# Optimization experiments

Hardware: AMD Instinct MI355X
Metric: run time of the kernel (lower is better)

Reference implementation:

```python
import jax, jax.numpy as jnp
import numpy as np

N, L, D1, D2, K, C, T = 50000, 1024, 512, 256, 64, 2, 49


def setup_inputs() -> dict:
    key = jax.random.key(0)
    ks = jax.random.split(key, 20)
    s = 0.02
    return {
        "h": jax.random.normal(ks[0], (N, L), dtype=jnp.float32),
        "tabular": jax.random.normal(ks[1], (1, T), dtype=jnp.float32),
        "label": 1,
        # fc: Linear(1024,512)+ReLU
        "W_fc": jax.random.normal(ks[2], (L, D1)) * s, "b_fc": jnp.zeros((D1,)),
        # gated attention net
        "Wa": jax.random.normal(ks[3], (D1, D2)) * s, "ba": jnp.zeros((D2,)),
        "Wb": jax.random.normal(ks[4], (D1, D2)) * s, "bb": jnp.zeros((D2,)),
        "Wc": jax.random.normal(ks[5], (D2, 1)) * s, "bc": jnp.zeros((1,)),
        # per-class instance classifiers Linear(512,2), stacked [C, D1, 2]
        "W_inst": jax.random.normal(ks[6], (C, D1, 2)) * s, "b_inst": jnp.zeros((C, 2)),
        # MultiHeadAttention (1 head)
        "W_img": jax.random.normal(ks[7], (D1, 1)) * s, "b_img": jnp.zeros((1,)),
        "W_tab": jax.random.normal(ks[8], (T, T)) * s, "b_tab": jnp.zeros((T,)),
        # bag classifier Linear(512+49, 2)
        "W_cls": jax.random.normal(ks[9], (D1 + T, C)) * s, "b_cls": jnp.zeros((C,)),
    }


def _forward(h, tabular, label, W_fc, b_fc, Wa, ba, Wb, bb, Wc, bc,
             W_inst, b_inst, W_img, b_img, W_tab, b_tab, W_cls, b_cls):
    # attention_net: fc + ReLU then gated attention
    h512 = jax.nn.relu(h @ W_fc + b_fc)                       # [N, 512]
    a = jnp.tanh(h512 @ Wa + ba)                              # [N, 256]
    b = jax.nn.sigmoid(h512 @ Wb + bb)                        # [N, 256]
    A = ((a * b) @ Wc + bc).T                                 # [1, N]
    A_raw = A
    A = jax.nn.softmax(A, axis=1)                             # [1, N]

    # instance eval: top-k positive / top-k negative selection + tiny classifier + CE
    scores = A[0]                                             # [N]
    _, top_p_ids = jax.lax.top_k(scores, K)
    _, top_n_ids = jax.lax.top_k(-scores, K)
    all_inst = jnp.concatenate([h512[top_p_ids], h512[top_n_ids]], axis=0)  # [2K, 512]
    targets = jnp.concatenate([jnp.ones((K,), jnp.int32), jnp.zeros((K,), jnp.int32)])

    def inst_loss(Wi, bi):
        logits = all_inst @ Wi + bi                           # [2K, 2]
        logp = jax.nn.log_softmax(logits, axis=1)
        return -jnp.mean(logp[jnp.arange(2 * K), targets])

    losses = jax.vmap(inst_loss)(W_inst, b_inst)              # [C]
    onehot = jax.nn.one_hot(label, C, dtype=losses.dtype)
    total_inst_loss = jnp.sum(onehot * losses)                # only in-class classifier contributes

    # attention pooling
    M = A @ h512                                              # [1, 512]

    # MultiHeadAttention (1 head): gated image feature + softmax-gated tabular feature
    img_score = jax.nn.sigmoid(M @ W_img + b_img)             # [1, 1]
    tab_score = jax.nn.softmax(tabular @ W_tab + b_tab, axis=1)  # [1, 49]
    concat = jnp.concatenate([img_score * M, tab_score * tabular], axis=1)  # [1, 561]

    logits = concat @ W_cls + b_cls                           # [1, 2]
    Y_prob = jax.nn.softmax(logits, axis=1)
    Y_hat = jnp.argmax(logits, axis=1)
    return logits, Y_prob, Y_hat, A_raw, total_inst_loss


def reference(h, tabular, label, W_fc, b_fc, Wa, ba, Wb, bb, Wc, bc,
              W_inst, b_inst, W_img, b_img, W_tab, b_tab, W_cls, b_cls):
    return _forward(h, tabular, label, W_fc, b_fc, Wa, ba, Wb, bb, Wc, bc,
                    W_inst, b_inst, W_img, b_img, W_tab, b_tab, W_cls, b_cls)
```

## Files before the change

kernel.cpp:

```cpp
#include <hip/hip_runtime.h>
#include <stdint.h>

typedef __bf16 bf16x8 __attribute__((ext_vector_type(8)));
typedef float f32x4 __attribute__((ext_vector_type(4)));
typedef unsigned short u16;
typedef unsigned int u32;

#define N_INST 50000
#define NPAD   50048
#define LIN    1024
#define D1     512
#define D2     256
#define TOPK   64
#define TDIM   49
#define NBIN   65536
#define CAND_MAX 8192
#define ZERO_DW (520 + 128 + 16 + NBIN)

__device__ __forceinline__ float b2f(u16 u) {
    union { float f; u32 i; } x; x.i = ((u32)u) << 16; return x.f;
}
__device__ __forceinline__ u16 f2b(float f) {
    union { float f; u32 i; } x; x.f = f;
    u32 r = x.i + 0x7FFFu + ((x.i >> 16) & 1u);
    return (u16)(r >> 16);
}
__device__ __forceinline__ void gload16(const void* g, void* l) {
    __builtin_amdgcn_global_load_lds((const __attribute__((address_space(1))) void*)g,
                                     (__attribute__((address_space(3))) void*)l, 16, 0, 0);
}

__global__ void pack_w(const float* __restrict__ W_fc, const float* __restrict__ Wa,
                       const float* __restrict__ Wb, u16* __restrict__ WfcT,
                       u16* __restrict__ WaT, u16* __restrict__ WbT, u32* __restrict__ zbase) {
    int gt = blockIdx.x * blockDim.x + threadIdx.x;
    int nthr = gridDim.x * blockDim.x;
    for (int z = gt; z < ZERO_DW; z += nthr) zbase[z] = 0u;
    for (int e = gt; e < D1 * LIN; e += nthr) {
        int n = e >> 10, k = e & 1023;
        WfcT[e] = f2b(W_fc[(size_t)k * D1 + n]);
    }
    for (int f = gt; f < D2 * D1; f += nthr) {
        int j = f >> 9, k = f & 511;
        WaT[f] = f2b(Wa[(size_t)k * D2 + j]);
        WbT[f] = f2b(Wb[(size_t)k * D2 + j]);
    }
}

__global__ __launch_bounds__(512, 2)
void gemm_fc(const float* __restrict__ h, const u16* __restrict__ WfcT,
             const float* __restrict__ b_fc, u16* __restrict__ h512) {
    __shared__ __align__(16) u16 lA[128 * 64];
    __shared__ __align__(16) u16 lB[512 * 64];
    const int tid = threadIdx.x;
    const int lane = tid & 63, wid = tid >> 6;
    const int wr = wid >> 2, wc = wid & 3;
    const int lanelo = lane & 15, lanehi = lane >> 4;
    const int row0 = blockIdx.x * 128;

    const int arow = tid >> 2;
    const int aseg = tid & 3;
    int srow = row0 + arow; if (srow >= N_INST) srow = N_INST - 1;
    const float* abase = h + (size_t)srow * LIN + aseg * 16;

    f32x4 acc[4][8];
    const f32x4 z4 = {0.f, 0.f, 0.f, 0.f};
    #pragma unroll
    for (int m = 0; m < 4; ++m)
        #pragma unroll
        for (int n = 0; n < 8; ++n) acc[m][n] = z4;

    for (int kt = 0; kt < LIN / 64; ++kt) {
        #pragma unroll
        for (int q = 0; q < 8; ++q) {
            int c = tid + 512 * q;
            int col = c >> 3, k8 = c & 7;
            gload16(WfcT + (size_t)col * LIN + kt * 64 + k8 * 8, (char*)lB + c * 16);
        }
        {
            const float4* ap = (const float4*)(abase + kt * 64);
            float4 a0 = ap[0], a1 = ap[1], a2 = ap[2], a3 = ap[3];
            bf16x8 w0, w1;
            w0[0] = (__bf16)a0.x; w0[1] = (__bf16)a0.y; w0[2] = (__bf16)a0.z; w0[3] = (__bf16)a0.w;
            w0[4] = (__bf16)a1.x; w0[5] = (__bf16)a1.y; w0[6] = (__bf16)a1.z; w0[7] = (__bf16)a1.w;
            w1[0] = (__bf16)a2.x; w1[1] = (__bf16)a2.y; w1[2] = (__bf16)a2.z; w1[3] = (__bf16)a2.w;
            w1[4] = (__bf16)a3.x; w1[5] = (__bf16)a3.y; w1[6] = (__bf16)a3.z; w1[7] = (__bf16)a3.w;
            *(bf16x8*)(lA + arow * 64 + aseg * 16) = w0;
            *(bf16x8*)(lA + arow * 64 + aseg * 16 + 8) = w1;
        }
        __syncthreads();
        #pragma unroll
        for (int kk = 0; kk < 2; ++kk) {
            bf16x8 af[4], bfr[8];
            #pragma unroll
            for (int m = 0; m < 4; ++m)
                af[m] = *(const bf16x8*)((char*)lA + (wr * 64 + m * 16 + lanelo) * 128 + kk * 64 + lanehi * 16);
            #pragma unroll
            for (int n = 0; n < 8; ++n)
                bfr[n] = *(const bf16x8*)((char*)lB + (wc * 128 + n * 16 + lanelo) * 128 + kk * 64 + lanehi * 16);
            #pragma unroll
            for (int m = 0; m < 4; ++m)
                #pragma unroll
                for (int n = 0; n < 8; ++n)
                    acc[m][n] = __builtin_amdgcn_mfma_f32_16x16x32_bf16(af[m], bfr[n], acc[m][n], 0, 0, 0);
        }
        __syncthreads();
    }
    #pragma unroll
    for (int n = 0; n < 8; ++n) {
        int col = wc * 128 + n * 16 + lanelo;
        float bias = b_fc[col];
        #pragma unroll
        for (int m = 0; m < 4; ++m) {
            int rbase = row0 + wr * 64 + m * 16 + 4 * lanehi;
            #pragma unroll
            for (int r = 0; r < 4; ++r) {
                float v = acc[m][n][r] + bias;
                v = v > 0.f ? v : 0.f;
                h512[(size_t)(rbase + r) * D1 + col] = f2b(v);
            }
        }
    }
}

__global__ __launch_bounds__(512, 2)
void gemm_attn(const u16* __restrict__ h512, const u16* __restrict__ WaT,
               const u16* __restrict__ WbT, const float* __restrict__ ba,
               const float* __restrict__ bb, const float* __restrict__ Wc,
               const float* __restrict__ bc, float* __restrict__ araw,
               u32* __restrict__ uarr, u32* __restrict__ hist,
               float* __restrict__ Zacc, float* __restrict__ Mpart) {
    __shared__ __align__(16) u16 lA[128 * 64];
    __shared__ __align__(16) u16 lBa[256 * 64];
    __shared__ __align__(16) u16 lBb[256 * 64];
    __shared__ float rsum[128];
    __shared__ float sW[128];
    const int tid = threadIdx.x;
    const int lane = tid & 63, wid = tid >> 6;
    const int wr = wid >> 2, wc4 = wid & 3;
    const int lanelo = lane & 15, lanehi = lane >> 4;
    const int row0 = blockIdx.x * 128;

    f32x4 accA[4][4], accB[4][4];
    const f32x4 z4 = {0.f, 0.f, 0.f, 0.f};
    for (int m = 0; m < 4; ++m)
        for (int n = 0; n < 4; ++n) { accA[m][n] = z4; accB[m][n] = z4; }

    for (int kt = 0; kt < D1 / 64; ++kt) {
        #pragma unroll
        for (int q = 0; q < 2; ++q) {
            int c = tid + 512 * q;
            int row = c >> 3, k8 = c & 7;
            gload16(h512 + (size_t)(row0 + row) * D1 + kt * 64 + k8 * 8, (char*)lA + c * 16);
        }
        #pragma unroll
        for (int q = 0; q < 4; ++q) {
            int c = tid + 512 * q;
            int col = c >> 3, k8 = c & 7;
            gload16(WaT + (size_t)col * D1 + kt * 64 + k8 * 8, (char*)lBa + c * 16);
            gload16(WbT + (size_t)col * D1 + kt * 64 + k8 * 8, (char*)lBb + c * 16);
        }
        __syncthreads();
        #pragma unroll
        for (int kk = 0; kk < 2; ++kk) {
            bf16x8 af[4], ga[4], gb[4];
            #pragma unroll
            for (int m = 0; m < 4; ++m)
                af[m] = *(const bf16x8*)((char*)lA + (wr * 64 + m * 16 + lanelo) * 128 + kk * 64 + lanehi * 16);
            #pragma unroll
            for (int n = 0; n < 4; ++n) {
                u32 off = (wc4 * 64 + n * 16 + lanelo) * 128 + kk * 64 + lanehi * 16;
                ga[n] = *(const bf16x8*)((char*)lBa + off);
                gb[n] = *(const bf16x8*)((char*)lBb + off);
            }
            #pragma unroll
            for (int m = 0; m < 4; ++m)
                #pragma unroll
                for (int n = 0; n < 4; ++n) {
                    accA[m][n] = __builtin_amdgcn_mfma_f32_16x16x32_bf16(af[m], ga[n], accA[m][n], 0, 0, 0);
                    accB[m][n] = __builtin_amdgcn_mfma_f32_16x16x32_bf16(af[m], gb[n], accB[m][n], 0, 0, 0);
                }
        }
        __syncthreads();
    }

    if (tid < 128) rsum[tid] = 0.f;
    __syncthreads();

    float baR[4], bbR[4], wcR[4];
    #pragma unroll
    for (int n = 0; n < 4; ++n) {
        int j = wc4 * 64 + n * 16 + lanelo;
        baR[n] = ba[j]; bbR[n] = bb[j]; wcR[n] = Wc[j];
    }
    #pragma unroll
    for (int m = 0; m < 4; ++m) {
        #pragma unroll
        for (int r = 0; r < 4; ++r) {
            float s = 0.f;
            #pragma unroll
            for (int n = 0; n < 4; ++n) {
                float av = accA[m][n][r] + baR[n];
                float bv = accB[m][n][r] + bbR[n];
                float p = tanhf(av) / (1.f + expf(-bv));
                s += p * wcR[n];
            }
            s += __shfl_xor(s, 1); s += __shfl_xor(s, 2);
            s += __shfl_xor(s, 4); s += __shfl_xor(s, 8);
            if (lanelo == 0) atomicAdd(&rsum[wr * 64 + m * 16 + 4 * lanehi + r], s);
        }
    }
    __syncthreads();

    if (tid < 128) {
        int rg = row0 + tid;
        float e = 0.f;
        if (rg < N_INST) {
            float a = rsum[tid] + bc[0];
            araw[rg] = a;
            u32 bits = __float_as_uint(a);
            u32 key = (bits & 0x80000000u) ? ~bits : (bits | 0x80000000u);
            uarr[rg] = key;
            atomicAdd(&hist[key >> 16], 1u);
            e = expf(a);
        }
        sW[tid] = e;
    }
    __syncthreads();
    if (tid < 128) {
        float e = sW[tid];
        for (int o = 32; o > 0; o >>= 1) e += __shfl_xor(e, o);
        if (lane == 0) atomicAdd(Zacc, e);
    }
    float accM = 0.f;
    for (int i = 0; i < 128; ++i)
        accM += sW[i] * b2f(h512[(size_t)(row0 + i) * D1 + tid]);
    atomicAdd(&Mpart[tid], accM);
}

__global__ void topk_collect(const u32* __restrict__ hist, const u32* __restrict__ uarr,
                             int* __restrict__ ctl, int* __restrict__ ids,
                             u32* __restrict__ cV0, int* __restrict__ cI0,
                             u32* __restrict__ cV1, int* __restrict__ cI1) {
    __shared__ int part[256];
    __shared__ int sp0, sb0, sp1, sb1;
    const int t = threadIdx.x;
    const uint4* h4 = (const uint4*)hist;
    int s = 0;
    for (int j = 0; j < 64; ++j) {
        uint4 v = h4[t * 64 + j];
        s += (int)(v.x + v.y + v.z + v.w);
    }
    part[t] = s;
    __syncthreads();
    for (int off = 1; off < 256; off <<= 1) {
        int v = part[t];
        int a = (t >= off) ? part[t - off] : 0;
        __syncthreads();
        part[t] = v + a;
        __syncthreads();
    }
    int run = part[t] - s;
    for (int j = 0; j < 64; ++j) {
        uint4 v = h4[t * 64 + j];
        int c4[4]; c4[0] = (int)v.x; c4[1] = (int)v.y; c4[2] = (int)v.z; c4[3] = (int)v.w;
        #pragma unroll
        for (int e = 0; e < 4; ++e) {
            int cnt = c4[e];
            if (cnt > 0) {
                int b = t * 256 + j * 4 + e;
                int less = run, greater = N_INST - run - cnt;
                if (greater < TOPK && greater + cnt >= TOPK) { sp0 = b; sb0 = greater; }
                if (less < TOPK && less + cnt >= TOPK)       { sp1 = b; sb1 = less; }
            }
            run += cnt;
        }
    }
    __syncthreads();
    const int p0 = sp0, p1 = sp1;
    if (blockIdx.x == 0 && t == 0) { ctl[0] = sp0; ctl[1] = sb0; ctl[2] = sp1; ctl[3] = sb1; }

    int gt = blockIdx.x * blockDim.x + t;
    int nthr = gridDim.x * blockDim.x;
    for (int i = gt; i < N_INST; i += nthr) {
        u32 v = uarr[i];
        int b = (int)(v >> 16);
        if (b > p0)       { int p = atomicAdd(&ctl[8], 1);  ids[p] = i; }
        else if (b == p0) { int p = atomicAdd(&ctl[9], 1);  if (p < CAND_MAX) { cV0[p] = v; cI0[p] = i; } }
        if (b < p1)       { int p = atomicAdd(&ctl[10], 1); ids[TOPK + p] = i; }
        else if (b == p1) { int p = atomicAdd(&ctl[11], 1); if (p < CAND_MAX) { cV1[p] = v; cI1[p] = i; } }
    }
}

__global__ void tail_fused(const int* __restrict__ ctl,
                           const u32* __restrict__ cV0, const int* __restrict__ cI0,
                           const u32* __restrict__ cV1, const int* __restrict__ cI1,
                           int* __restrict__ ids, const u16* __restrict__ h512,
                           const float* __restrict__ W_inst, const float* __restrict__ b_inst,
                           const int* __restrict__ label, const float* __restrict__ Mpart,
                           const float* __restrict__ Zacc, const float* __restrict__ tabular,
                           const float* __restrict__ W_img, const float* __restrict__ b_img,
                           const float* __restrict__ W_tab, const float* __restrict__ b_tab,
                           const float* __restrict__ W_cls, const float* __restrict__ b_cls,
                           float* __restrict__ d_out) {
    __shared__ int h8[256];
    __shared__ int eq[2048];
    __shared__ int s_d1, s_k1, s_d2, s_fill, s_eqc;
    __shared__ float lsum;
    __shared__ float sM[512];
    __shared__ float stab[TDIM];
    __shared__ float red0[256], red1[256];
    __shared__ float simg;
    const int tid = threadIdx.x;
    const int lane = tid & 63, wid = tid >> 6;

    for (int mode = 0; mode < 2; ++mode) {
        int basem = ctl[mode * 2 + 1];
        int need = TOPK - basem;
        int ccnt = ctl[9 + mode * 2];
        if (ccnt > CAND_MAX) ccnt = CAND_MAX;
        const u32* cV = mode ? cV1 : cV0;
        const int* cI = mode ? cI1 : cI0;
        int* dst = ids + mode * TOPK;
        h8[tid] = 0; __syncthreads();
        for (int i = tid; i < ccnt; i += 256) atomicAdd(&h8[(cV[i] >> 8) & 255u], 1);
        __syncthreads();
        if (tid == 0) {
            int acc = 0, d, k = need;
            if (mode == 0) { for (d = 255; d >= 0; --d) { acc += h8[d]; if (acc >= k) break; } }
            else           { for (d = 0; d < 256; ++d)  { acc += h8[d]; if (acc >= k) break; } }
            s_d1 = d; s_k1 = k - (acc - h8[d]);
        }
        __syncthreads();
        int d1 = s_d1, k1 = s_k1;
        h8[tid] = 0; __syncthreads();
        for (int i = tid; i < ccnt; i += 256) {
            u32 v = cV[i];
            if (((v >> 8) & 255u) == (u32)d1) atomicAdd(&h8[v & 255u], 1);
        }
        __syncthreads();
        if (tid == 0) {
            int acc = 0, d, k = k1;
            if (mode == 0) { for (d = 255; d >= 0; --d) { acc += h8[d]; if (acc >= k) break; } }
            else           { for (d = 0; d < 256; ++d)  { acc += h8[d]; if (acc >= k) break; } }
            s_d2 = d; s_fill = 0; s_eqc = 0;
        }
        __syncthreads();
        u32 vth = ((u32)ctl[mode * 2] << 16) | ((u32)d1 << 8) | (u32)s_d2;
        for (int i = tid; i < ccnt; i += 256) {
            u32 v = cV[i];
            bool better = mode == 0 ? (v > vth) : (v < vth);
            if (better)        { int p = atomicAdd(&s_fill, 1); dst[basem + p] = cI[i]; }
            else if (v == vth) { int p = atomicAdd(&s_eqc, 1);  if (p < 2048) eq[p] = cI[i]; }
        }
        __syncthreads();
        if (tid == 0) {
            int have = basem + s_fill;
            int rem = TOPK - have;
            int m = s_eqc < 2048 ? s_eqc : 2048;
            int last = -1;
            for (int q = 0; q < rem; ++q) {
                int best = 0x7FFFFFFF;
                for (int s = 0; s < m; ++s) { int ix = eq[s]; if (ix > last && ix < best) best = ix; }
                dst[have + q] = best; last = best;
            }
        }
        __syncthreads();
    }

    if (tid == 0) lsum = 0.f;
    __syncthreads();
    const int lab = label[0];
    const float* W = W_inst + (size_t)lab * (D1 * 2);
    const float b0 = b_inst[lab * 2 + 0], b1 = b_inst[lab * 2 + 1];
    for (int i = 0; i < 32; ++i) {
        int r = wid * 32 + i;
        int row = ids[r];
        float s0 = 0.f, s1 = 0.f;
        for (int s = 0; s < 8; ++s) {
            int j = lane + 64 * s;
            float hv = b2f(h512[(size_t)row * D1 + j]);
            s0 += hv * W[j * 2 + 0];
            s1 += hv * W[j * 2 + 1];
        }
        for (int o = 32; o > 0; o >>= 1) { s0 += __shfl_xor(s0, o); s1 += __shfl_xor(s1, o); }
        if (lane == 0) {
            float l0 = s0 + b0, l1 = s1 + b1;
            float mx = fmaxf(l0, l1);
            float lse = mx + logf(expf(l0 - mx) + expf(l1 - mx));
            float lt = (r < TOPK) ? l1 : l0;
            atomicAdd(&lsum, lse - lt);
        }
    }
    __syncthreads();
    if (tid == 0) d_out[50005] = lsum / 128.f;

    float invZ = 1.f / Zacc[0];
    sM[tid] = Mpart[tid] * invZ;
    sM[tid + 256] = Mpart[tid + 256] * invZ;
    red0[tid] = sM[tid] * W_img[tid] + sM[tid + 256] * W_img[tid + 256];
    __syncthreads();
    for (int o = 128; o > 0; o >>= 1) { if (tid < o) red0[tid] += red0[tid + o]; __syncthreads(); }
    if (tid == 0) simg = 1.f / (1.f + expf(-(red0[0] + b_img[0])));
    if (tid < TDIM) {
        float t = b_tab[tid];
        for (int kx = 0; kx < TDIM; ++kx) t += tabular[kx] * W_tab[kx * TDIM + tid];
        stab[tid] = t;
    }
    __syncthreads();
    if (tid == 0) {
        float mx = stab[0];
        for (int o = 1; o < TDIM; ++o) mx = fmaxf(mx, stab[o]);
        float ss = 0.f;
        for (int o = 0; o < TDIM; ++o) { float e = expf(stab[o] - mx); stab[o] = e; ss += e; }
        for (int o = 0; o < TDIM; ++o) stab[o] = (stab[o] / ss) * tabular[o];
    }
    __syncthreads();
    float img = simg;
    float a0 = 0.f, a1 = 0.f;
    for (int j = tid; j < D1 + TDIM; j += 256) {
        float w = (j < D1) ? img * sM[j] : stab[j - D1];
        a0 += w * W_cls[j * 2 + 0];
        a1 += w * W_cls[j * 2 + 1];
    }
    red0[tid] = a0; red1[tid] = a1;
    __syncthreads();
    for (int o = 128; o > 0; o >>= 1) {
        if (tid < o) { red0[tid] += red0[tid + o]; red1[tid] += red1[tid + o]; }
        __syncthreads();
    }
    if (tid == 0) {
        float l0 = red0[0] + b_cls[0];
        float l1 = red1[0] + b_cls[1];
        d_out[0] = l0; d_out[1] = l1;
        float mx = fmaxf(l0, l1);
        float e0 = expf(l0 - mx), e1 = expf(l1 - mx);
        d_out[2] = e0 / (e0 + e1);
        d_out[3] = e1 / (e0 + e1);
        d_out[4] = (l1 > l0) ? 1.f : 0.f;
    }
}

extern "C" void kernel_launch(void* const* d_in, const int* in_sizes, int n_in,
                              void* d_out, int out_size, void* d_ws, size_t ws_size,
                              hipStream_t stream) {
    const float* h       = (const float*)d_in[0];
    const float* tabular = (const float*)d_in[1];
    const int*   label   = (const int*)d_in[2];
    const float* W_fc    = (const float*)d_in[3];
    const float* b_fc    = (const float*)d_in[4];
    const float* Wa      = (const float*)d_in[5];
    const float* ba      = (const float*)d_in[6];
    const float* Wb      = (const float*)d_in[7];
    const float* bb      = (const float*)d_in[8];
    const float* Wc      = (const float*)d_in[9];
    const float* bc      = (const float*)d_in[10];
    const float* W_inst  = (const float*)d_in[11];
    const float* b_inst  = (const float*)d_in[12];
    const float* W_img   = (const float*)d_in[13];
    const float* b_img   = (const float*)d_in[14];
    const float* W_tab   = (const float*)d_in[15];
    const float* b_tab   = (const float*)d_in[16];
    const float* W_cls   = (const float*)d_in[17];
    const float* b_cls   = (const float*)d_in[18];
    float* out = (float*)d_out;

    u16* h512 = (u16*)d_ws;
    u16* WfcT = h512 + (size_t)NPAD * D1;
    u16* WaT  = WfcT + (size_t)D1 * LIN;
    u16* WbT  = WaT + (size_t)D2 * D1;
    u32* uarr = (u32*)(WbT + (size_t)D2 * D1);
    float* accum = (float*)(uarr + NPAD);
    float* Zacc  = accum;
    float* Mpart = accum + 8;
    int* ids = (int*)(accum + 8 + D1);
    int* ctl = ids + 128;
    u32* hist = (u32*)(ctl + 16);
    u32* cV0 = hist + NBIN;
    int* cI0 = (int*)(cV0 + CAND_MAX);
    u32* cV1 = (u32*)(cI0 + CAND_MAX);
    int* cI1 = (int*)(cV1 + CAND_MAX);

    pack_w<<<dim3(256), dim3(256), 0, stream>>>(W_fc, Wa, Wb, WfcT, WaT, WbT, (u32*)accum);
    gemm_fc<<<dim3(NPAD / 128), dim3(512), 0, stream>>>(h, WfcT, b_fc, h512);
    gemm_attn<<<dim3(NPAD / 128), dim3(512), 0, stream>>>(
        h512, WaT, WbT, ba, bb, Wc, bc, out + 5, uarr, hist, Zacc, Mpart);
    topk_collect<<<dim3(128), dim3(256), 0, stream>>>(hist, uarr, ctl, ids, cV0, cI0, cV1, cI1);
    tail_fused<<<dim3(1), dim3(256), 0, stream>>>(
        ctl, cV0, cI0, cV1, cI1, ids, h512, W_inst, b_inst, label,
        Mpart, Zacc, tabular, W_img, b_img, W_tab, b_tab, W_cls, b_cls, out);
}
```

Baseline: 319.5 us.

## Swizzle LDS layouts, split fc GEMM columns, prefetch A tile into registers

Applies an XOR swizzle to the LDS tile layout in both GEMMs so the MFMA fragment reads avoid bank conflicts. The fc GEMM is split into two column halves on a 2D grid, cutting per-block LDS and accumulator registers, and the next A tile is prefetched into registers while MFMAs run. The trade-off is that the fp32 input h is now read and converted twice, once per column half, raising global traffic on the largest input.

```diff
diff --git a/kernel.cpp b/kernel.cpp
--- a/kernel.cpp
+++ b/kernel.cpp
@@ -29,6 +29,9 @@
     __builtin_amdgcn_global_load_lds((const __attribute__((address_space(1))) void*)g,
                                      (__attribute__((address_space(3))) void*)l, 16, 0, 0);
 }
+__device__ __forceinline__ u32 swz(int row, int bytecol) {
+    return (u32)(row * 128 + (bytecol ^ ((row & 7) << 4)));
+}
 
 __global__ void pack_w(const float* __restrict__ W_fc, const float* __restrict__ Wa,
                        const float* __restrict__ Wb, u16* __restrict__ WfcT,
@@ -51,64 +54,77 @@
 void gemm_fc(const float* __restrict__ h, const u16* __restrict__ WfcT,
              const float* __restrict__ b_fc, u16* __restrict__ h512) {
     __shared__ __align__(16) u16 lA[128 * 64];
-    __shared__ __align__(16) u16 lB[512 * 64];
+    __shared__ __align__(16) u16 lB[256 * 64];
     const int tid = threadIdx.x;
     const int lane = tid & 63, wid = tid >> 6;
     const int wr = wid >> 2, wc = wid & 3;
     const int lanelo = lane & 15, lanehi = lane >> 4;
-    const int row0 = blockIdx.x * 128;
+    const int row0 = blockIdx.y * 128;
+    const int col0 = blockIdx.x * 256;
 
     const int arow = tid >> 2;
     const int aseg = tid & 3;
     int srow = row0 + arow; if (srow >= N_INST) srow = N_INST - 1;
     const float* abase = h + (size_t)srow * LIN + aseg * 16;
-
-    f32x4 acc[4][8];
+    u16* aw0 = (u16*)((char*)lA + swz(arow, aseg * 32));
+    u16* aw1 = (u16*)((char*)lA + swz(arow, aseg * 32 + 16));
+
+    f32x4 acc[4][4];
     const f32x4 z4 = {0.f, 0.f, 0.f, 0.f};
     #pragma unroll
     for (int m = 0; m < 4; ++m)
         #pragma unroll
-        for (int n = 0; n < 8; ++n) acc[m][n] = z4;
+        for (int n = 0; n < 4; ++n) acc[m][n] = z4;
+
+    float4 a0, a1, a2, a3;
+    { const float4* ap = (const float4*)abase; a0 = ap[0]; a1 = ap[1]; a2 = ap[2]; a3 = ap[3]; }
 
     for (int kt = 0; kt < LIN / 64; ++kt) {
         #pragma unroll
-        for (int q = 0; q < 8; ++q) {
+        for (int q = 0; q < 4; ++q) {
             int c = tid + 512 * q;
-            int col = c >> 3, k8 = c & 7;
-            gload16(WfcT + (size_t)col * LIN + kt * 64 + k8 * 8, (char*)lB + c * 16);
+            int col = c >> 3, d8 = c & 7;
+            int k8 = d8 ^ (col & 7);
+            gload16(WfcT + (size_t)(col0 + col) * LIN + kt * 64 + k8 * 8, (char*)lB + c * 16);
         }
         {
-            const float4* ap = (const float4*)(abase + kt * 64);
-            float4 a0 = ap[0], a1 = ap[1], a2 = ap[2], a3 = ap[3];
             bf16x8 w0, w1;
             w0[0] = (__bf16)a0.x; w0[1] = (__bf16)a0.y; w0[2] = (__bf16)a0.z; w0[3] = (__bf16)a0.w;
             w0[4] = (__bf16)a1.x; w0[5] = (__bf16)a1.y; w0[6] = (__bf16)a1.z; w0[7] = (__bf16)a1.w;
             w1[0] = (__bf16)a2.x; w1[1] = (__bf16)a2.y; w1[2] = (__bf16)a2.z; w1[3] = (__bf16)a2.w;
             w1[4] = (__bf16)a3.x; w1[5] = (__bf16)a3.y; w1[6] = (__bf16)a3.z; w1[7] = (__bf16)a3.w;
-            *(bf16x8*)(lA + arow * 64 + aseg * 16) = w0;
-            *(bf16x8*)(lA + arow * 64 + aseg * 16 + 8) = w1;
-        }
-        __syncthreads();
+            *(bf16x8*)aw0 = w0;
+            *(bf16x8*)aw1 = w1;
+        }
+        __syncthreads();
+        if (kt + 1 < LIN / 64) {
+            const float4* ap = (const float4*)(abase + (kt + 1) * 64);
+            a0 = ap[0]; a1 = ap[1]; a2 = ap[2]; a3 = ap[3];
+        }
         #pragma unroll
         for (int kk = 0; kk < 2; ++kk) {
-            bf16x8 af[4], bfr[8];
-            #pragma unroll
-            for (int m = 0; m < 4; ++m)
-                af[m] = *(const bf16x8*)((char*)lA + (wr * 64 + m * 16 + lanelo) * 128 + kk * 64 + lanehi * 16);
-            #pragma unroll
-            for (int n = 0; n < 8; ++n)
-                bfr[n] = *(const bf16x8*)((char*)lB + (wc * 128 + n * 16 + lanelo) * 128 + kk * 64 + lanehi * 16);
+            bf16x8 af[4], bfr[4];
+            #pragma unroll
+            for (int m = 0; m < 4; ++m) {
+                int row = wr * 64 + m * 16 + lanelo;
+                af[m] = *(const bf16x8*)((char*)lA + swz(row, kk * 64 + lanehi * 16));
+            }
+            #pragma unroll
+            for (int n = 0; n < 4; ++n) {
+                int col = wc * 64 + n * 16 + lanelo;
+                bfr[n] = *(const bf16x8*)((char*)lB + swz(col, kk * 64 + lanehi * 16));
+            }
             #pragma unroll
             for (int m = 0; m < 4; ++m)
                 #pragma unroll
-                for (int n = 0; n < 8; ++n)
+                for (int n = 0; n < 4; ++n)
                     acc[m][n] = __builtin_amdgcn_mfma_f32_16x16x32_bf16(af[m], bfr[n], acc[m][n], 0, 0, 0);
         }
         __syncthreads();
     }
     #pragma unroll
-    for (int n = 0; n < 8; ++n) {
-        int col = wc * 128 + n * 16 + lanelo;
+    for (int n = 0; n < 4; ++n) {
+        int col = col0 + wc * 64 + n * 16 + lanelo;
         float bias = b_fc[col];
         #pragma unroll
         for (int m = 0; m < 4; ++m) {
@@ -150,13 +166,15 @@
         #pragma unroll
         for (int q = 0; q < 2; ++q) {
             int c = tid + 512 * q;
-            int row = c >> 3, k8 = c & 7;
+            int row = c >> 3, d8 = c & 7;
+            int k8 = d8 ^ (row & 7);
             gload16(h512 + (size_t)(row0 + row) * D1 + kt * 64 + k8 * 8, (char*)lA + c * 16);
         }
         #pragma unroll
         for (int q = 0; q < 4; ++q) {
             int c = tid + 512 * q;
-            int col = c >> 3, k8 = c & 7;
+            int col = c >> 3, d8 = c & 7;
+            int k8 = d8 ^ (col & 7);
             gload16(WaT + (size_t)col * D1 + kt * 64 + k8 * 8, (char*)lBa + c * 16);
             gload16(WbT + (size_t)col * D1 + kt * 64 + k8 * 8, (char*)lBb + c * 16);
         }
@@ -165,11 +183,14 @@
         for (int kk = 0; kk < 2; ++kk) {
             bf16x8 af[4], ga[4], gb[4];
             #pragma unroll
-            for (int m = 0; m < 4; ++m)
-                af[m] = *(const bf16x8*)((char*)lA + (wr * 64 + m * 16 + lanelo) * 128 + kk * 64 + lanehi * 16);
+            for (int m = 0; m < 4; ++m) {
+                int row = wr * 64 + m * 16 + lanelo;
+                af[m] = *(const bf16x8*)((char*)lA + swz(row, kk * 64 + lanehi * 16));
+            }
             #pragma unroll
             for (int n = 0; n < 4; ++n) {
-                u32 off = (wc4 * 64 + n * 16 + lanelo) * 128 + kk * 64 + lanehi * 16;
+                int col = wc4 * 64 + n * 16 + lanelo;
+                u32 off = swz(col, kk * 64 + lanehi * 16);
                 ga[n] = *(const bf16x8*)((char*)lBa + off);
                 gb[n] = *(const bf16x8*)((char*)lBb + off);
             }
@@ -482,7 +503,7 @@
     int* cI1 = (int*)(cV1 + CAND_MAX);
 
     pack_w<<<dim3(256), dim3(256), 0, stream>>>(W_fc, Wa, Wb, WfcT, WaT, WbT, (u32*)accum);
-    gemm_fc<<<dim3(NPAD / 128), dim3(512), 0, stream>>>(h, WfcT, b_fc, h512);
+    gemm_fc<<<dim3(2, NPAD / 128), dim3(512), 0, stream>>>(h, WfcT, b_fc, h512);
     gemm_attn<<<dim3(NPAD / 128), dim3(512), 0, stream>>>(
         h512, WaT, WbT, ba, bb, Wc, bc, out + 5, uarr, hist, Zacc, Mpart);
     topk_collect<<<dim3(128), dim3(256), 0, stream>>>(hist, uarr, ctl, ids, cV0, cI0, cV1, cI1);
```

New measurement: 308.7 us. 3.4% less time.
